# Kernel tuning notes

Measured on AMD Instinct MI355X. Metric: run time of the kernel, lower is better.

Reference implementation:

```python
import jax, jax.numpy as jnp
import numpy as np
from jax import lax

EPS = 1e-5
NEG_SLOPE = 0.01

def setup_inputs() -> dict:
    key = jax.random.key(0)
    ks = jax.random.split(key, 9)
    B, Cin, Cout, D, H, W = 2, 32, 64, 20, 20, 20
    x = jax.random.normal(ks[0], (B, Cin, D, H, W), dtype=jnp.float32)
    conv_w = jax.random.normal(ks[1], (Cout, Cin, 3, 3, 3), dtype=jnp.float32) * 0.05
    conv_b = jnp.zeros((Cout,), dtype=jnp.float32)
    gamma = jnp.ones((Cout,), dtype=jnp.float32)
    beta = jnp.zeros((Cout,), dtype=jnp.float32)
    wq = jax.random.normal(ks[2], (Cout, Cout), dtype=jnp.float32) * 0.05
    bq = jnp.zeros((Cout,), dtype=jnp.float32)
    wk = jax.random.normal(ks[3], (Cout, Cout), dtype=jnp.float32) * 0.05
    bk = jnp.zeros((Cout,), dtype=jnp.float32)
    wv = jax.random.normal(ks[4], (Cout, Cout), dtype=jnp.float32) * 0.05
    bv = jnp.zeros((Cout,), dtype=jnp.float32)
    return {"x": x, "conv_w": conv_w, "conv_b": conv_b, "gamma": gamma,
            "beta": beta, "wq": wq, "bq": bq, "wk": wk, "bk": bk,
            "wv": wv, "bv": bv}

def reference(x, conv_w, conv_b, gamma, beta, wq, bq, wk, bk, wv, bv):
    # Conv3d k=3, stride=1, padding=1 (SAME)
    y = lax.conv_general_dilated(
        x, conv_w, window_strides=(1, 1, 1), padding='SAME',
        dimension_numbers=('NCDHW', 'OIDHW', 'NCDHW'))
    y = y + conv_b[None, :, None, None, None]
    # InstanceNorm3d: normalize over spatial dims per (batch, channel)
    mu = jnp.mean(y, axis=(2, 3, 4), keepdims=True)
    var = jnp.mean(jnp.square(y - mu), axis=(2, 3, 4), keepdims=True)
    y = (y - mu) * lax.rsqrt(var + EPS)
    y = y * gamma[None, :, None, None, None] + beta[None, :, None, None, None]
    # LeakyReLU
    y = jnp.where(y >= 0, y, NEG_SLOPE * y)
    # Attention: 1x1x1 convs -> flatten -> bmm softmax bmm (no scaling)
    B, C, D, H, W = y.shape
    N = D * H * W
    f = y.reshape(B, C, N)                                  # [B, C, N]
    q = jnp.einsum('oc,bcn->bon', wq, f) + bq[None, :, None]
    k = jnp.einsum('oc,bcn->bon', wk, f) + bk[None, :, None]
    v = jnp.einsum('oc,bcn->bon', wv, f) + bv[None, :, None]
    att = jax.nn.softmax(jnp.einsum('bcn,bcm->bnm', q, k), axis=-1)  # [B,N,N]
    out = jnp.einsum('bck,bqk->bcq', v, att)                # [B, C, N]
    return out.reshape(B, C, D, H, W)
```

## Files before the change

### kernel.cpp

```cpp
#include <hip/hip_runtime.h>
#include <math.h>

#define CIN   32
#define COUT  64
#define DD    20
#define PD    22
#define PSP   (PD*PD*PD)
#define NSP   8000
#define BB    2
#define EPSN  1e-5f
#define SLOPE 0.01f
#define LOG2E 1.4426950408889634f

#define NT     250
#define SPLITS 8
#define QUADS  63

#define COG 4
#define OG  8

typedef float  f32x16 __attribute__((ext_vector_type(16)));
typedef short  short8 __attribute__((ext_vector_type(8)));

__device__ __forceinline__ unsigned short f2bf_rne(float x) {
    unsigned u = __float_as_uint(x);
    unsigned r = (u + 0x7FFFu + ((u >> 16) & 1u)) >> 16;
    return (unsigned short)r;
}
__device__ __forceinline__ float bf2f(unsigned short h) {
    return __uint_as_float(((unsigned)h) << 16);
}
__device__ __forceinline__ short8 ld_frag(const unsigned short* p) {
    uint4 t = *reinterpret_cast<const uint4*>(p);
    return __builtin_bit_cast(short8, t);
}
__device__ __forceinline__ void gload_lds16(const void* gsrc, void* ldst) {
    typedef __attribute__((address_space(1))) const unsigned int GU;
    typedef __attribute__((address_space(3))) unsigned int LU;
    __builtin_amdgcn_global_load_lds((GU*)gsrc, (LU*)ldst, 16, 0, 0);
}
__device__ __forceinline__ float exp2_fast(float x) {
    float r;
    asm("v_exp_f32 %0, %1" : "=v"(r) : "v"(x));
    return r;
}
__device__ __forceinline__ float wsum(float x) {
    #pragma unroll
    for (int off = 1; off < 64; off <<= 1) x += __shfl_xor(x, off, 64);
    return x;
}

__global__ void pad_k(const float* __restrict__ x, float* __restrict__ xp) {
    int idx = blockIdx.x * blockDim.x + threadIdx.x;
    if (idx >= BB * CIN * PSP) return;
    int pw = idx % PD;
    int ph = (idx / PD) % PD;
    int pd = (idx / (PD * PD)) % PD;
    int bc = idx / PSP;
    float v = 0.f;
    if (pw >= 1 && pw <= DD && ph >= 1 && ph <= DD && pd >= 1 && pd <= DD)
        v = x[(size_t)bc * NSP + ((size_t)(pd - 1) * DD + (ph - 1)) * DD + (pw - 1)];
    xp[idx] = v;
}

__global__ __launch_bounds__(256) void conv3d_k(const float* __restrict__ xp,
                                                const float* __restrict__ w,
                                                const float* __restrict__ bias,
                                                float* __restrict__ y,
                                                float2* __restrict__ part) {
    int blk = blockIdx.x;
    int vb  = blk & 31;
    int cg  = (blk >> 5) & 15;
    int b   = blk >> 9;
    int vox = vb * 256 + threadIdx.x;
    bool valid = vox < NSP;
    int v  = valid ? vox : 0;
    int w_ = v % DD;
    int h_ = (v / DD) % DD;
    int d_ = v / (DD * DD);
    int pvox = ((d_ + 1) * PD + (h_ + 1)) * PD + (w_ + 1);
    const float* xb = xp + (size_t)b * CIN * PSP + pvox;

    float acc[COG];
    #pragma unroll
    for (int j = 0; j < COG; ++j) acc[j] = 0.f;

    for (int ci = 0; ci < CIN; ++ci) {
        const float* xc = xb + (size_t)ci * PSP;
        float xv[27];
        #pragma unroll
        for (int kd = 0; kd < 3; ++kd)
            #pragma unroll
            for (int kh = 0; kh < 3; ++kh)
                #pragma unroll
                for (int kw = 0; kw < 3; ++kw)
                    xv[(kd * 3 + kh) * 3 + kw] =
                        xc[(kd - 1) * (PD * PD) + (kh - 1) * PD + (kw - 1)];
        #pragma unroll
        for (int j = 0; j < COG; ++j) {
            int co = cg * COG + j;
            const float* wr = w + ((size_t)co * CIN + ci) * 27;
            float a = acc[j];
            #pragma unroll
            for (int t = 0; t < 27; ++t) a += xv[t] * wr[t];
            acc[j] = a;
        }
    }

    __shared__ float2 wred[4][COG];
    int wv = threadIdx.x >> 6;
    int ln = threadIdx.x & 63;
    #pragma unroll
    for (int j = 0; j < COG; ++j) {
        int co = cg * COG + j;
        float val = valid ? acc[j] + bias[co] : 0.f;
        if (valid) y[((size_t)b * COUT + co) * NSP + vox] = val;
        float s  = wsum(val);
        float ss = wsum(val * val);
        if (ln == 0) wred[wv][j] = make_float2(s, ss);
    }
    __syncthreads();
    if (threadIdx.x < COG) {
        int j = threadIdx.x;
        float s = 0.f, ss = 0.f;
        #pragma unroll
        for (int w2 = 0; w2 < 4; ++w2) { s += wred[w2][j].x; ss += wred[w2][j].y; }
        part[((size_t)(b * COUT + cg * COG + j)) * 32 + vb] = make_float2(s, ss);
    }
}

__global__ __launch_bounds__(256) void qkv_k(const float* __restrict__ yraw,
                      const float2* __restrict__ part,
                      const float* __restrict__ gamma, const float* __restrict__ beta,
                      const float* __restrict__ wq, const float* __restrict__ bq,
                      const float* __restrict__ wk, const float* __restrict__ bk,
                      const float* __restrict__ wv, const float* __restrict__ bv,
                      unsigned short* __restrict__ Qfh,
                      unsigned short* __restrict__ Kfh,
                      unsigned short* __restrict__ Vf) {
    int blk = blockIdx.x;
    int vb  = blk & 31;
    int og  = (blk >> 5) & 7;
    int b   = blk >> 8;
    int n   = vb * 256 + threadIdx.x;
    bool valid = n < NSP;
    int nn  = valid ? n : 0;
    const float* fb = yraw + (size_t)b * COUT * NSP + nn;

    __shared__ float smean[COUT], srstd[COUT];
    if (threadIdx.x < COUT) {
        int c = threadIdx.x;
        float s = 0.f, ss = 0.f;
        #pragma unroll 8
        for (int ch = 0; ch < 32; ++ch) {
            float2 p = part[(size_t)(b * COUT + c) * 32 + ch];
            s += p.x; ss += p.y;
        }
        float mean = s * (1.f / NSP);
        smean[c] = mean;
        srstd[c] = rsqrtf(ss * (1.f / NSP) - mean * mean + EPSN);
    }
    __syncthreads();

    float aq[OG], ak[OG], av[OG];
    #pragma unroll
    for (int j = 0; j < OG; ++j) {
        int o = og * OG + j;
        aq[j] = bq[o]; ak[j] = bk[o]; av[j] = bv[o];
    }
    for (int c = 0; c < COUT; ++c) {
        float fc = (fb[(size_t)c * NSP] - smean[c]) * srstd[c] * gamma[c] + beta[c];
        fc = fc >= 0.f ? fc : SLOPE * fc;
        #pragma unroll
        for (int j = 0; j < OG; ++j) {
            int o = og * OG + j;
            aq[j] += wq[o * COUT + c] * fc;
            ak[j] += wk[o * COUT + c] * fc;
            av[j] += wv[o * COUT + c] * fc;
        }
    }
    if (!valid) return;

    int t  = n >> 5;
    int kk = n & 31;
    unsigned short qh[OG], kh[OG];
    #pragma unroll
    for (int j = 0; j < OG; ++j) {
        qh[j] = f2bf_rne(aq[j] * LOG2E);
        kh[j] = f2bf_rne(ak[j]);
    }
    size_t qko = ((size_t)((b * NT + t) * 4 + (og >> 1)) * 2 + (og & 1)) * 256 + kk * 8;
    *reinterpret_cast<uint4*>(Qfh + qko) = *reinterpret_cast<const uint4*>(qh);
    *reinterpret_cast<uint4*>(Kfh + qko) = *reinterpret_cast<const uint4*>(kh);
    {
        int Y = kk >> 4, hf = (kk >> 3) & 1, e = kk & 7;
        size_t vbase = ((size_t)((b * NT + t) * 2 + Y) * 2 + (og >> 2)) * 512
                     + hf * 256 + e;
        #pragma unroll
        for (int j = 0; j < OG; ++j)
            Vf[vbase + ((og & 3) * 8 + j) * 8] = f2bf_rne(av[j]);
    }
}

__global__ __launch_bounds__(256, 4) void attn_pass1_mfma(
        const unsigned short* __restrict__ Qfh,
        const unsigned short* __restrict__ Kfh,
        const unsigned short* __restrict__ Vf,
        float* __restrict__ pm, float* __restrict__ pl, float* __restrict__ pacc) {
    int bid   = blockIdx.x;
    int split = bid / (BB * QUADS);
    int rem   = bid % (BB * QUADS);
    int b     = rem / QUADS;
    int quad  = rem % QUADS;
    int wave  = threadIdx.x >> 6;
    int lane  = threadIdx.x & 63;
    int col   = lane & 31;
    int half  = lane >> 5;
    int qt    = quad * 4 + wave;
    bool qvalid = qt < NT;
    int qtc   = qvalid ? qt : NT - 1;
    int bNT   = b * NT;

    int tstart = (split * NT) / SPLITS;
    int tend   = ((split + 1) * NT) / SPLITS;
    int nkt    = tend - tstart;

    __shared__ __align__(16) char ldsbuf[3][8192];

    short8 qfh[4];
    {
        const unsigned short* qp = Qfh + (size_t)(bNT + qtc) * 2048 + lane * 8;
        #pragma unroll
        for (int c = 0; c < 4; ++c) qfh[c] = ld_frag(qp + c * 512);
    }

    int wo = wave * 1024;
    int go = wo + lane * 16;

    auto STAGE = [&](int bufi, int tg) {
        size_t tb = (size_t)(bNT + tg) * 2048;
        char* l = &ldsbuf[bufi][0];
        gload_lds16((const char*)(Kfh + tb) + go, l + wo);
        gload_lds16((const char*)(Vf  + tb) + go, l + 4096 + wo);
    };

    f32x16 oacc0 = {};
    f32x16 oacc1 = {};
    float m = -3e38f, lsum = 0.f;

    STAGE(0, tstart);
    STAGE(1, tstart + 1);

    for (int t = 0; t < nkt; ++t) {
        if (t == nkt - 1) { asm volatile("s_waitcnt vmcnt(0)" ::: "memory"); }
        else              { asm volatile("s_waitcnt vmcnt(2)" ::: "memory"); }
        __builtin_amdgcn_sched_barrier(0);
        __builtin_amdgcn_s_barrier();
        __builtin_amdgcn_sched_barrier(0);
        if (t + 2 < nkt) STAGE((t + 2) % 3, tstart + t + 2);

        const unsigned short* lk = (const unsigned short*)&ldsbuf[t % 3][0];
        const unsigned short* lv = (const unsigned short*)&ldsbuf[t % 3][4096];

        f32x16 s = {};
        __builtin_amdgcn_s_setprio(1);
        #pragma unroll
        for (int c = 0; c < 4; ++c) {
            short8 kfh = ld_frag(lk + c * 512 + lane * 8);
            s = __builtin_amdgcn_mfma_f32_32x32x16_bf16(kfh, qfh[c], s, 0, 0, 0);
        }
        __builtin_amdgcn_s_setprio(0);

        float a0 = fmaxf(fmaxf(s[0],  s[1]),  s[2]);
        float a1 = fmaxf(fmaxf(s[3],  s[4]),  s[5]);
        float a2 = fmaxf(fmaxf(s[6],  s[7]),  s[8]);
        float a3 = fmaxf(fmaxf(s[9],  s[10]), s[11]);
        float a4 = fmaxf(fmaxf(s[12], s[13]), s[14]);
        float tmax = fmaxf(fmaxf(fmaxf(a0, a1), a2), fmaxf(fmaxf(a3, a4), s[15]));
        tmax = fmaxf(tmax, __shfl_xor(tmax, 32, 64));
        if (__any(tmax > m + 11.5f)) {
            float newm  = fmaxf(m, tmax);
            float scale = exp2_fast(m - newm);
            lsum *= scale;
            #pragma unroll
            for (int r = 0; r < 16; ++r) { oacc0[r] *= scale; oacc1[r] *= scale; }
            m = newm;
        }
        short8 pf0, pf1;
        float ls;
        {
            float p[8];
            #pragma unroll
            for (int r = 0; r < 8; ++r) p[r] = exp2_fast(s[r] - m);
            ls = ((p[0] + p[1]) + (p[2] + p[3])) + ((p[4] + p[5]) + (p[6] + p[7]));
            unsigned W[4], X[4];
            #pragma unroll
            for (int j = 0; j < 4; ++j)
                asm("v_cvt_pk_bf16_f32 %0, %1, %2" : "=v"(W[j]) : "v"(p[2 * j]), "v"(p[2 * j + 1]));
            #pragma unroll
            for (int j = 0; j < 4; ++j) X[j] = (unsigned)__shfl_xor((int)W[j], 32, 64);
            uint4 u = half ? make_uint4(X[2], X[3], W[2], W[3])
                           : make_uint4(W[0], W[1], X[0], X[1]);
            pf0 = __builtin_bit_cast(short8, u);
        }
        {
            float p[8];
            #pragma unroll
            for (int r = 0; r < 8; ++r) p[r] = exp2_fast(s[r + 8] - m);
            ls += ((p[0] + p[1]) + (p[2] + p[3])) + ((p[4] + p[5]) + (p[6] + p[7]));
            unsigned W[4], X[4];
            #pragma unroll
            for (int j = 0; j < 4; ++j)
                asm("v_cvt_pk_bf16_f32 %0, %1, %2" : "=v"(W[j]) : "v"(p[2 * j]), "v"(p[2 * j + 1]));
            #pragma unroll
            for (int j = 0; j < 4; ++j) X[j] = (unsigned)__shfl_xor((int)W[j], 32, 64);
            uint4 u = half ? make_uint4(X[2], X[3], W[2], W[3])
                           : make_uint4(W[0], W[1], X[0], X[1]);
            pf1 = __builtin_bit_cast(short8, u);
        }
        lsum += ls;
        {
            short8 v00 = ld_frag(lv + 0 * 512 + lane * 8);
            short8 v10 = ld_frag(lv + 1 * 512 + lane * 8);
            __builtin_amdgcn_s_setprio(1);
            oacc0 = __builtin_amdgcn_mfma_f32_32x32x16_bf16(v00, pf0, oacc0, 0, 0, 0);
            oacc1 = __builtin_amdgcn_mfma_f32_32x32x16_bf16(v10, pf0, oacc1, 0, 0, 0);
            __builtin_amdgcn_s_setprio(0);
            short8 v01 = ld_frag(lv + 2 * 512 + lane * 8);
            short8 v11 = ld_frag(lv + 3 * 512 + lane * 8);
            __builtin_amdgcn_s_setprio(1);
            oacc0 = __builtin_amdgcn_mfma_f32_32x32x16_bf16(v01, pf1, oacc0, 0, 0, 0);
            oacc1 = __builtin_amdgcn_mfma_f32_32x32x16_bf16(v11, pf1, oacc1, 0, 0, 0);
            __builtin_amdgcn_s_setprio(0);
        }
    }

    if (!qvalid) return;
    int q0 = qt * 32;
    float lfull = lsum + __shfl_xor(lsum, 32, 64);
    size_t base = (size_t)b * SPLITS + split;
    if (lane < 32) {
        pm[base * NSP + q0 + col] = m;
        pl[base * NSP + q0 + col] = lfull;
    }
    float* pa = pacc + base * (size_t)(COUT * NSP) + q0 + col;
    #pragma unroll
    for (int r = 0; r < 16; ++r) {
        int crow = (r & 3) + 8 * (r >> 2) + 4 * half;
        pa[(size_t)crow * NSP]        = oacc0[r];
        pa[(size_t)(crow + 32) * NSP] = oacc1[r];
    }
}

__global__ void attn_combine_k(const float* __restrict__ pm, const float* __restrict__ pl,
                               const float* __restrict__ pacc, float* __restrict__ out) {
    int idx = blockIdx.x * blockDim.x + threadIdx.x;
    const int N4 = NSP / 4;
    if (idx >= BB * COUT * N4) return;
    int n4 = idx % N4;
    int c  = (idx / N4) % COUT;
    int b  = idx / (N4 * COUT);
    int n  = n4 * 4;

    float4 M = make_float4(-1e30f, -1e30f, -1e30f, -1e30f);
    #pragma unroll
    for (int j = 0; j < SPLITS; ++j) {
        float4 v = *reinterpret_cast<const float4*>(&pm[((size_t)b * SPLITS + j) * NSP + n]);
        M.x = fmaxf(M.x, v.x); M.y = fmaxf(M.y, v.y);
        M.z = fmaxf(M.z, v.z); M.w = fmaxf(M.w, v.w);
    }
    float4 L = make_float4(0.f, 0.f, 0.f, 0.f);
    float4 O = make_float4(0.f, 0.f, 0.f, 0.f);
    #pragma unroll
    for (int j = 0; j < SPLITS; ++j) {
        size_t base = (size_t)b * SPLITS + j;
        float4 pmv = *reinterpret_cast<const float4*>(&pm[base * NSP + n]);
        float4 plv = *reinterpret_cast<const float4*>(&pl[base * NSP + n]);
        float4 pav = *reinterpret_cast<const float4*>(&pacc[(base * COUT + c) * NSP + n]);
        float4 wgt;
        wgt.x = exp2_fast(pmv.x - M.x); wgt.y = exp2_fast(pmv.y - M.y);
        wgt.z = exp2_fast(pmv.z - M.z); wgt.w = exp2_fast(pmv.w - M.w);
        L.x += plv.x * wgt.x; L.y += plv.y * wgt.y;
        L.z += plv.z * wgt.z; L.w += plv.w * wgt.w;
        O.x += pav.x * wgt.x; O.y += pav.y * wgt.y;
        O.z += pav.z * wgt.z; O.w += pav.w * wgt.w;
    }
    float4 r;
    r.x = O.x / L.x; r.y = O.y / L.y; r.z = O.z / L.z; r.w = O.w / L.w;
    *reinterpret_cast<float4*>(&out[((size_t)(b * COUT + c)) * NSP + n]) = r;
}

extern "C" void kernel_launch(void* const* d_in, const int* in_sizes, int n_in,
                              void* d_out, int out_size, void* d_ws, size_t ws_size,
                              hipStream_t stream) {
    const float* x      = (const float*)d_in[0];
    const float* conv_w = (const float*)d_in[1];
    const float* conv_b = (const float*)d_in[2];
    const float* gamma  = (const float*)d_in[3];
    const float* beta   = (const float*)d_in[4];
    const float* wq     = (const float*)d_in[5];
    const float* bq     = (const float*)d_in[6];
    const float* wk     = (const float*)d_in[7];
    const float* bk     = (const float*)d_in[8];
    const float* wv     = (const float*)d_in[9];
    const float* bv     = (const float*)d_in[10];
    float* out = (float*)d_out;

    const int ELEMS = BB * COUT * NSP;
    char* w8 = (char*)d_ws;
    float*  y    = (float*)w8;
    float2* part = (float2*)(w8 + 4096000);
    unsigned short* Qfh = (unsigned short*)(w8 + 4128768);
    unsigned short* Kfh = Qfh + (size_t)ELEMS;
    unsigned short* Vf  = Kfh + (size_t)ELEMS;
    float* pm   = (float*)(Vf + (size_t)ELEMS);
    float* pl   = pm + (size_t)BB * SPLITS * NSP;
    float* pacc = pl + (size_t)BB * SPLITS * NSP;
    float* xpad = pacc;

    pad_k<<<(BB * CIN * PSP + 255) / 256, 256, 0, stream>>>(x, xpad);
    conv3d_k<<<BB * 16 * 32, 256, 0, stream>>>(xpad, conv_w, conv_b, y, part);
    qkv_k<<<BB * 8 * 32, 256, 0, stream>>>(y, part, gamma, beta,
                                           wq, bq, wk, bk, wv, bv,
                                           Qfh, Kfh, Vf);
    attn_pass1_mfma<<<SPLITS * BB * QUADS, 256, 0, stream>>>(Qfh, Kfh, Vf,
                                                             pm, pl, pacc);
    attn_combine_k<<<(BB * COUT * (NSP / 4) + 255) / 256, 256, 0, stream>>>(pm, pl, pacc, out);
}
```

Measured before the change: 134.6 us.

## Process key/value tiles in pairs with double-buffered LDS stages

The attention loop now handles two K/V tiles per iteration. It uses two 16KB LDS buffers, each holding a pair of tiles, in place of the three-slot single-tile ring. This halves the number of block barriers per key range and exposes two independent QK MFMA chains before the softmax/PV step, which should improve MFMA issue overlap. The explicit vmcnt-based wait is replaced by __syncthreads, so every barrier may wait for all outstanding loads. The effective prefetch distance is also reduced to one pair, which risks exposing load latency. A tail path handles an odd tile count.

```diff
diff --git a/kernel.cpp b/kernel.cpp
--- a/kernel.cpp
+++ b/kernel.cpp
@@ -224,8 +224,10 @@
     int tstart = (split * NT) / SPLITS;
     int tend   = ((split + 1) * NT) / SPLITS;
     int nkt    = tend - tstart;
-
-    __shared__ __align__(16) char ldsbuf[3][8192];
+    int npair  = nkt >> 1;
+    int odd    = nkt & 1;
+
+    __shared__ __align__(16) char ldsbuf[2][16384];
 
     short8 qfh[4];
     {
@@ -237,9 +239,9 @@
     int wo = wave * 1024;
     int go = wo + lane * 16;
 
-    auto STAGE = [&](int bufi, int tg) {
+    auto STAGET = [&](int bufi, int slot, int tg) {
         size_t tb = (size_t)(bNT + tg) * 2048;
-        char* l = &ldsbuf[bufi][0];
+        char* l = &ldsbuf[bufi][slot * 8192];
         gload_lds16((const char*)(Kfh + tb) + go, l + wo);
         gload_lds16((const char*)(Vf  + tb) + go, l + 4096 + wo);
     };
@@ -248,29 +250,7 @@
     f32x16 oacc1 = {};
     float m = -3e38f, lsum = 0.f;
 
-    STAGE(0, tstart);
-    STAGE(1, tstart + 1);
-
-    for (int t = 0; t < nkt; ++t) {
-        if (t == nkt - 1) { asm volatile("s_waitcnt vmcnt(0)" ::: "memory"); }
-        else              { asm volatile("s_waitcnt vmcnt(2)" ::: "memory"); }
-        __builtin_amdgcn_sched_barrier(0);
-        __builtin_amdgcn_s_barrier();
-        __builtin_amdgcn_sched_barrier(0);
-        if (t + 2 < nkt) STAGE((t + 2) % 3, tstart + t + 2);
-
-        const unsigned short* lk = (const unsigned short*)&ldsbuf[t % 3][0];
-        const unsigned short* lv = (const unsigned short*)&ldsbuf[t % 3][4096];
-
-        f32x16 s = {};
-        __builtin_amdgcn_s_setprio(1);
-        #pragma unroll
-        for (int c = 0; c < 4; ++c) {
-            short8 kfh = ld_frag(lk + c * 512 + lane * 8);
-            s = __builtin_amdgcn_mfma_f32_32x32x16_bf16(kfh, qfh[c], s, 0, 0, 0);
-        }
-        __builtin_amdgcn_s_setprio(0);
-
+    auto SM_PV = [&](const f32x16& s, const unsigned short* lv) {
         float a0 = fmaxf(fmaxf(s[0],  s[1]),  s[2]);
         float a1 = fmaxf(fmaxf(s[3],  s[4]),  s[5]);
         float a2 = fmaxf(fmaxf(s[6],  s[7]),  s[8]);
@@ -319,20 +299,67 @@
             pf1 = __builtin_bit_cast(short8, u);
         }
         lsum += ls;
-        {
-            short8 v00 = ld_frag(lv + 0 * 512 + lane * 8);
-            short8 v10 = ld_frag(lv + 1 * 512 + lane * 8);
-            __builtin_amdgcn_s_setprio(1);
-            oacc0 = __builtin_amdgcn_mfma_f32_32x32x16_bf16(v00, pf0, oacc0, 0, 0, 0);
-            oacc1 = __builtin_amdgcn_mfma_f32_32x32x16_bf16(v10, pf0, oacc1, 0, 0, 0);
-            __builtin_amdgcn_s_setprio(0);
-            short8 v01 = ld_frag(lv + 2 * 512 + lane * 8);
-            short8 v11 = ld_frag(lv + 3 * 512 + lane * 8);
-            __builtin_amdgcn_s_setprio(1);
-            oacc0 = __builtin_amdgcn_mfma_f32_32x32x16_bf16(v01, pf1, oacc0, 0, 0, 0);
-            oacc1 = __builtin_amdgcn_mfma_f32_32x32x16_bf16(v11, pf1, oacc1, 0, 0, 0);
-            __builtin_amdgcn_s_setprio(0);
-        }
+        short8 v00 = ld_frag(lv + 0 * 512 + lane * 8);
+        short8 v10 = ld_frag(lv + 1 * 512 + lane * 8);
+        __builtin_amdgcn_s_setprio(1);
+        oacc0 = __builtin_amdgcn_mfma_f32_32x32x16_bf16(v00, pf0, oacc0, 0, 0, 0);
+        oacc1 = __builtin_amdgcn_mfma_f32_32x32x16_bf16(v10, pf0, oacc1, 0, 0, 0);
+        __builtin_amdgcn_s_setprio(0);
+        short8 v01 = ld_frag(lv + 2 * 512 + lane * 8);
+        short8 v11 = ld_frag(lv + 3 * 512 + lane * 8);
+        __builtin_amdgcn_s_setprio(1);
+        oacc0 = __builtin_amdgcn_mfma_f32_32x32x16_bf16(v01, pf1, oacc0, 0, 0, 0);
+        oacc1 = __builtin_amdgcn_mfma_f32_32x32x16_bf16(v11, pf1, oacc1, 0, 0, 0);
+        __builtin_amdgcn_s_setprio(0);
+    };
+
+    STAGET(0, 0, tstart);
+    STAGET(0, 1, tstart + 1);
+
+    for (int p = 0; p < npair; ++p) {
+        __syncthreads();
+        int nb = (p + 1) & 1;
+        if (p + 1 < npair) {
+            STAGET(nb, 0, tstart + 2 * p + 2);
+            STAGET(nb, 1, tstart + 2 * p + 3);
+        } else if (odd) {
+            STAGET(nb, 0, tstart + 2 * p + 2);
+        }
+        const unsigned short* base = (const unsigned short*)&ldsbuf[p & 1][0];
+        const unsigned short* lk0 = base;
+        const unsigned short* lv0 = base + 2048;
+        const unsigned short* lk1 = base + 4096;
+        const unsigned short* lv1 = base + 6144;
+
+        f32x16 s0 = {}, s1 = {};
+        __builtin_amdgcn_s_setprio(1);
+        #pragma unroll
+        for (int c = 0; c < 4; ++c) {
+            short8 k0 = ld_frag(lk0 + c * 512 + lane * 8);
+            s0 = __builtin_amdgcn_mfma_f32_32x32x16_bf16(k0, qfh[c], s0, 0, 0, 0);
+        }
+        #pragma unroll
+        for (int c = 0; c < 4; ++c) {
+            short8 k1 = ld_frag(lk1 + c * 512 + lane * 8);
+            s1 = __builtin_amdgcn_mfma_f32_32x32x16_bf16(k1, qfh[c], s1, 0, 0, 0);
+        }
+        __builtin_amdgcn_s_setprio(0);
+
+        SM_PV(s0, lv0);
+        SM_PV(s1, lv1);
+    }
+    if (odd) {
+        __syncthreads();
+        const unsigned short* base = (const unsigned short*)&ldsbuf[npair & 1][0];
+        f32x16 s0 = {};
+        __builtin_amdgcn_s_setprio(1);
+        #pragma unroll
+        for (int c = 0; c < 4; ++c) {
+            short8 k0 = ld_frag(base + c * 512 + lane * 8);
+            s0 = __builtin_amdgcn_mfma_f32_32x32x16_bf16(k0, qfh[c], s0, 0, 0, 0);
+        }
+        __builtin_amdgcn_s_setprio(0);
+        SM_PV(s0, base + 2048);
     }
 
     if (!qvalid) return;
```

Measured after the change: 133.1 us. Within noise of the previous version (-1.1%).

## Drop LDS staging in attention; one-wave blocks load K/V directly

Applied to the files above, without the earlier changes.

The attention pass previously ran 4 waves per block that shared K/V tiles through a triple-buffered LDS pipeline with async global-to-LDS loads and barriers. Each block is now a single wave handling one query tile and loading its K/V fragments straight from global memory into registers, which removes the barriers and the padded quad logic. The QKV projection is also split into twice as many blocks, each computing 4 output channels, to raise parallelism. In exchange, K/V tiles are no longer shared across waves in a block and must come from L2/cache per wave, with no explicit prefetch to hide load latency.

```diff
diff --git a/kernel.cpp b/kernel.cpp
--- a/kernel.cpp
+++ b/kernel.cpp
@@ -14,10 +14,9 @@
 
 #define NT     250
 #define SPLITS 8
-#define QUADS  63
 
 #define COG 4
-#define OG  8
+#define OG  4
 
 typedef float  f32x16 __attribute__((ext_vector_type(16)));
 typedef short  short8 __attribute__((ext_vector_type(8)));
@@ -33,11 +32,6 @@
 __device__ __forceinline__ short8 ld_frag(const unsigned short* p) {
     uint4 t = *reinterpret_cast<const uint4*>(p);
     return __builtin_bit_cast(short8, t);
-}
-__device__ __forceinline__ void gload_lds16(const void* gsrc, void* ldst) {
-    typedef __attribute__((address_space(1))) const unsigned int GU;
-    typedef __attribute__((address_space(3))) unsigned int LU;
-    __builtin_amdgcn_global_load_lds((GU*)gsrc, (LU*)ldst, 16, 0, 0);
 }
 __device__ __forceinline__ float exp2_fast(float x) {
     float r;
@@ -140,8 +134,8 @@
                       unsigned short* __restrict__ Vf) {
     int blk = blockIdx.x;
     int vb  = blk & 31;
-    int og  = (blk >> 5) & 7;
-    int b   = blk >> 8;
+    int og  = (blk >> 5) & 15;
+    int b   = blk >> 9;
     int n   = vb * 256 + threadIdx.x;
     bool valid = n < NSP;
     int nn  = valid ? n : 0;
@@ -189,86 +183,67 @@
         qh[j] = f2bf_rne(aq[j] * LOG2E);
         kh[j] = f2bf_rne(ak[j]);
     }
-    size_t qko = ((size_t)((b * NT + t) * 4 + (og >> 1)) * 2 + (og & 1)) * 256 + kk * 8;
-    *reinterpret_cast<uint4*>(Qfh + qko) = *reinterpret_cast<const uint4*>(qh);
-    *reinterpret_cast<uint4*>(Kfh + qko) = *reinterpret_cast<const uint4*>(kh);
+    size_t qko = ((size_t)((b * NT + t) * 4 + (og >> 2)) * 2 + ((og >> 1) & 1)) * 256
+               + kk * 8 + (og & 1) * 4;
+    *reinterpret_cast<uint2*>(Qfh + qko) = *reinterpret_cast<const uint2*>(qh);
+    *reinterpret_cast<uint2*>(Kfh + qko) = *reinterpret_cast<const uint2*>(kh);
     {
         int Y = kk >> 4, hf = (kk >> 3) & 1, e = kk & 7;
-        size_t vbase = ((size_t)((b * NT + t) * 2 + Y) * 2 + (og >> 2)) * 512
+        size_t vbase = ((size_t)((b * NT + t) * 2 + Y) * 2 + (og >> 3)) * 512
                      + hf * 256 + e;
         #pragma unroll
         for (int j = 0; j < OG; ++j)
-            Vf[vbase + ((og & 3) * 8 + j) * 8] = f2bf_rne(av[j]);
-    }
-}
-
-__global__ __launch_bounds__(256, 4) void attn_pass1_mfma(
+            Vf[vbase + ((og & 7) * 4 + j) * 8] = f2bf_rne(av[j]);
+    }
+}
+
+__global__ __launch_bounds__(64, 4) void attn_pass1_mfma(
         const unsigned short* __restrict__ Qfh,
         const unsigned short* __restrict__ Kfh,
         const unsigned short* __restrict__ Vf,
         float* __restrict__ pm, float* __restrict__ pl, float* __restrict__ pacc) {
     int bid   = blockIdx.x;
-    int split = bid / (BB * QUADS);
-    int rem   = bid % (BB * QUADS);
-    int b     = rem / QUADS;
-    int quad  = rem % QUADS;
-    int wave  = threadIdx.x >> 6;
-    int lane  = threadIdx.x & 63;
+    int split = bid / (BB * NT);
+    int rem   = bid % (BB * NT);
+    int b     = rem / NT;
+    int qt    = rem % NT;
+    int lane  = threadIdx.x;
     int col   = lane & 31;
     int half  = lane >> 5;
-    int qt    = quad * 4 + wave;
-    bool qvalid = qt < NT;
-    int qtc   = qvalid ? qt : NT - 1;
     int bNT   = b * NT;
 
     int tstart = (split * NT) / SPLITS;
     int tend   = ((split + 1) * NT) / SPLITS;
-    int nkt    = tend - tstart;
-
-    __shared__ __align__(16) char ldsbuf[3][8192];
 
     short8 qfh[4];
     {
-        const unsigned short* qp = Qfh + (size_t)(bNT + qtc) * 2048 + lane * 8;
+        const unsigned short* qp = Qfh + (size_t)(bNT + qt) * 2048 + lane * 8;
         #pragma unroll
         for (int c = 0; c < 4; ++c) qfh[c] = ld_frag(qp + c * 512);
     }
-
-    int wo = wave * 1024;
-    int go = wo + lane * 16;
-
-    auto STAGE = [&](int bufi, int tg) {
-        size_t tb = (size_t)(bNT + tg) * 2048;
-        char* l = &ldsbuf[bufi][0];
-        gload_lds16((const char*)(Kfh + tb) + go, l + wo);
-        gload_lds16((const char*)(Vf  + tb) + go, l + 4096 + wo);
-    };
 
     f32x16 oacc0 = {};
     f32x16 oacc1 = {};
     float m = -3e38f, lsum = 0.f;
 
-    STAGE(0, tstart);
-    STAGE(1, tstart + 1);
-
-    for (int t = 0; t < nkt; ++t) {
-        if (t == nkt - 1) { asm volatile("s_waitcnt vmcnt(0)" ::: "memory"); }
-        else              { asm volatile("s_waitcnt vmcnt(2)" ::: "memory"); }
-        __builtin_amdgcn_sched_barrier(0);
-        __builtin_amdgcn_s_barrier();
-        __builtin_amdgcn_sched_barrier(0);
-        if (t + 2 < nkt) STAGE((t + 2) % 3, tstart + t + 2);
-
-        const unsigned short* lk = (const unsigned short*)&ldsbuf[t % 3][0];
-        const unsigned short* lv = (const unsigned short*)&ldsbuf[t % 3][4096];
+    for (int t = tstart; t < tend; ++t) {
+        const unsigned short* kp = Kfh + (size_t)(bNT + t) * 2048 + lane * 8;
+        const unsigned short* vp = Vf  + (size_t)(bNT + t) * 2048 + lane * 8;
+        short8 kf0 = ld_frag(kp);
+        short8 kf1 = ld_frag(kp + 512);
+        short8 kf2 = ld_frag(kp + 1024);
+        short8 kf3 = ld_frag(kp + 1536);
+        short8 v00 = ld_frag(vp);
+        short8 v10 = ld_frag(vp + 512);
+        short8 v01 = ld_frag(vp + 1024);
+        short8 v11 = ld_frag(vp + 1536);
 
         f32x16 s = {};
         __builtin_amdgcn_s_setprio(1);
-        #pragma unroll
-        for (int c = 0; c < 4; ++c) {
-            short8 kfh = ld_frag(lk + c * 512 + lane * 8);
-            s = __builtin_amdgcn_mfma_f32_32x32x16_bf16(kfh, qfh[c], s, 0, 0, 0);
-        }
+        s = __builtin_amdgcn_mfma_f32_32x32x16_bf16(kf0, qfh[0], s, 0, 0, 0);
+        s = __builtin_amdgcn_mfma_f32_32x32x16_bf16(kf1, qfh[1], s, 0, 0, 0);
+        s = __builtin_amdgcn_mfma_f32_32x32x16_bf16(kf2, qfh[2], s, 0, 0, 0);
+        s = __builtin_amdgcn_mfma_f32_32x32x16_bf16(kf3, qfh[3], s, 0, 0, 0);
         __builtin_amdgcn_s_setprio(0);
 
         float a0 = fmaxf(fmaxf(s[0],  s[1]),  s[2]);
@@ -319,23 +294,14 @@
             pf1 = __builtin_bit_cast(short8, u);
         }
         lsum += ls;
-        {
-            short8 v00 = ld_frag(lv + 0 * 512 + lane * 8);
-            short8 v10 = ld_frag(lv + 1 * 512 + lane * 8);
-            __builtin_amdgcn_s_setprio(1);
-            oacc0 = __builtin_amdgcn_mfma_f32_32x32x16_bf16(v00, pf0, oacc0, 0, 0, 0);
-            oacc1 = __builtin_amdgcn_mfma_f32_32x32x16_bf16(v10, pf0, oacc1, 0, 0, 0);
-            __builtin_amdgcn_s_setprio(0);
-            short8 v01 = ld_frag(lv + 2 * 512 + lane * 8);
-            short8 v11 = ld_frag(lv + 3 * 512 + lane * 8);
-            __builtin_amdgcn_s_setprio(1);
-            oacc0 = __builtin_amdgcn_mfma_f32_32x32x16_bf16(v01, pf1, oacc0, 0, 0, 0);
-            oacc1 = __builtin_amdgcn_mfma_f32_32x32x16_bf16(v11, pf1, oacc1, 0, 0, 0);
-            __builtin_amdgcn_s_setprio(0);
-        }
-    }
-
-    if (!qvalid) return;
+        __builtin_amdgcn_s_setprio(1);
+        oacc0 = __builtin_amdgcn_mfma_f32_32x32x16_bf16(v00, pf0, oacc0, 0, 0, 0);
+        oacc1 = __builtin_amdgcn_mfma_f32_32x32x16_bf16(v10, pf0, oacc1, 0, 0, 0);
+        oacc0 = __builtin_amdgcn_mfma_f32_32x32x16_bf16(v01, pf1, oacc0, 0, 0, 0);
+        oacc1 = __builtin_amdgcn_mfma_f32_32x32x16_bf16(v11, pf1, oacc1, 0, 0, 0);
+        __builtin_amdgcn_s_setprio(0);
+    }
+
     int q0 = qt * 32;
     float lfull = lsum + __shfl_xor(lsum, 32, 64);
     size_t base = (size_t)b * SPLITS + split;
@@ -420,10 +386,10 @@
 
     pad_k<<<(BB * CIN * PSP + 255) / 256, 256, 0, stream>>>(x, xpad);
     conv3d_k<<<BB * 16 * 32, 256, 0, stream>>>(xpad, conv_w, conv_b, y, part);
-    qkv_k<<<BB * 8 * 32, 256, 0, stream>>>(y, part, gamma, beta,
-                                           wq, bq, wk, bk, wv, bv,
-                                           Qfh, Kfh, Vf);
-    attn_pass1_mfma<<<SPLITS * BB * QUADS, 256, 0, stream>>>(Qfh, Kfh, Vf,
-                                                             pm, pl, pacc);
+    qkv_k<<<BB * 16 * 32, 256, 0, stream>>>(y, part, gamma, beta,
+                                            wq, bq, wk, bk, wv, bv,
+                                            Qfh, Kfh, Vf);
+    attn_pass1_mfma<<<SPLITS * BB * NT, 64, 0, stream>>>(Qfh, Kfh, Vf,
+                                                         pm, pl, pacc);
     attn_combine_k<<<(BB * COUT * (NSP / 4) + 255) / 256, 256, 0, stream>>>(pm, pl, pacc, out);
 }
```

After: 133.8 us. No clear change (-0.6%).
